# Performance work log

Measured on AMD Instinct MI355X. Metric: run time of the kernel, lower is better.

Reference implementation:

```python
import jax, jax.numpy as jnp
import numpy as np

B, N, L, C, H = 2, 1024, 4096, 256, 8
D = C // H  # head_dim = 32


def setup_inputs() -> dict:
    root = jax.random.key(0)
    ks = jax.random.split(root, 16)
    s = 0.02  # init scale for weights
    return {
        "query": jax.random.normal(ks[0], (B, N, C), jnp.float32),
        "key": jax.random.normal(ks[1], (B, L, C), jnp.float32),
        "value": jax.random.normal(ks[2], (B, L, C), jnp.float32),
        "key_padding_mask": jnp.zeros((B, L), jnp.bool_),  # unused by forward
        "hw_lvl": 1,  # unused by forward
        # learned params, stored as [in, out] (i.e. torch weight transposed)
        "Wq": jax.random.normal(ks[3], (C, C), jnp.float32) * s,
        "Wk": jax.random.normal(ks[4], (C, C), jnp.float32) * s,
        "Wv": jax.random.normal(ks[5], (C, C), jnp.float32) * s,
        "Wp": jax.random.normal(ks[6], (C, C), jnp.float32) * s,
        "bp": jax.random.normal(ks[7], (C,), jnp.float32) * s,
        "Wl1": jax.random.normal(ks[8], (H, H), jnp.float32) * s,
        "bl1": jax.random.normal(ks[9], (H,), jnp.float32) * s,
        "Wl2": jax.random.normal(ks[10], (H, 1), jnp.float32) * s,
        "bl2": jax.random.normal(ks[11], (1,), jnp.float32) * s,
    }


def reference(query, key, value, key_padding_mask, hw_lvl,
              Wq, Wk, Wv, Wp, bp, Wl1, bl1, Wl2, bl2):
    b, n, c = query.shape
    l = key.shape[1]
    h = Wl1.shape[0]
    d = c // h
    scale = d ** (-0.5)

    # projections -> [B, H, N|L, D]
    q = (query @ Wq).reshape(b, n, h, d).transpose(0, 2, 1, 3)
    k = (key @ Wk).reshape(b, l, h, d).transpose(0, 2, 1, 3)
    v = (value @ Wv).reshape(b, l, h, d).transpose(0, 2, 1, 3)

    # raw attention scores [B, H, N, L]
    attn = jnp.einsum('bhnd,bhld->bhnl', q, k) * scale

    # tiny per-head MLP on scores: [B, N, L, H] -> ReLU(H->H) -> ReLU(H->1)
    attn_p = attn.transpose(0, 2, 3, 1)  # [B, N, L, H]
    new_feats = jax.nn.relu(attn_p @ Wl1 + bl1)
    mask = jax.nn.relu(new_feats @ Wl2 + bl2)  # [B, N, L, 1]

    # standard softmax-attention path on the raw scores
    p = jax.nn.softmax(attn, axis=-1)  # [B, H, N, L]
    x = jnp.einsum('bhnl,bhld->bhnd', p, v)  # [B, H, N, D]
    x = x.transpose(0, 2, 1, 3).reshape(b, n, c)
    x = x @ Wp + bp
    return (x, mask)
```

## Files before the change

kernel.cpp:

```cpp
#include <hip/hip_runtime.h>
#include <math.h>
#include <stdint.h>

typedef __bf16 bf16;
typedef __bf16 bfx8 __attribute__((ext_vector_type(8)));
typedef __bf16 bfx4 __attribute__((ext_vector_type(4)));
typedef short  sh8  __attribute__((ext_vector_type(8)));
typedef float  fx4  __attribute__((ext_vector_type(4)));
typedef _Float16 h2 __attribute__((ext_vector_type(2)));
typedef _Float16 hx4 __attribute__((ext_vector_type(4)));
typedef _Float16 h8 __attribute__((ext_vector_type(8)));

#define B_ 2
#define N_ 1024
#define L_ 4096
#define C_ 256
#define H_ 8
#define D_ 32
#define KL 32
#define LOG2E 1.4426950408889634f
#define LN2 0.6931471805599453f
#define QSCALE (0.17677669529663687f * LOG2E)

__device__ __forceinline__ float exp2fast(float x) {
    float r; asm("v_exp_f32 %0, %1" : "=v"(r) : "v"(x)); return r;
}
__device__ __forceinline__ _Float16 exp2h(_Float16 x) {
    _Float16 r; asm("v_exp_f16 %0, %1" : "=v"(r) : "v"(x)); return r;
}
__device__ __forceinline__ h2 pkrtz(float a, float b) {
    return __builtin_bit_cast(h2, __builtin_amdgcn_cvt_pkrtz(a, b));
}

__global__ __launch_bounds__(256)
void wtrans_kernel(const float* __restrict__ Wq, const float* __restrict__ Wk,
                   const float* __restrict__ Wv, const float* __restrict__ Wp,
                   const float* __restrict__ Wl1, const float* __restrict__ bl1,
                   const float* __restrict__ Wl2,
                   bf16* __restrict__ WTq, bf16* __restrict__ WTk,
                   bf16* __restrict__ WTv, bf16* __restrict__ WTp,
                   h2* __restrict__ mlpc) {
    const int bid = blockIdx.x;
    const int wsel = bid >> 4;
    const int tile = bid & 15;
    const int k0 = (tile >> 2) * 64;
    const int c0 = (tile & 3) * 64;
    const float* W = wsel == 0 ? Wq : wsel == 1 ? Wk : wsel == 2 ? Wv : Wp;
    bf16* WT = wsel == 0 ? WTq : wsel == 1 ? WTk : wsel == 2 ? WTv : WTp;

    __shared__ float t_lds[64][68];
    const int tid = threadIdx.x;
    if (bid == 0) {
        if (tid < 32) {
            const int hh = tid >> 2, jp = tid & 3;
            mlpc[tid] = (h2){(_Float16)(LN2 * Wl1[hh * 8 + 2 * jp]),
                             (_Float16)(LN2 * Wl1[hh * 8 + 2 * jp + 1])};
        }
        if (tid < 4) {
            mlpc[32 + tid] = (h2){(_Float16)bl1[2 * tid], (_Float16)bl1[2 * tid + 1]};
            mlpc[36 + tid] = (h2){(_Float16)Wl2[2 * tid], (_Float16)Wl2[2 * tid + 1]};
        }
    }
    {
        const int r = tid >> 2;
        const int c4 = (tid & 3) * 16;
        const float4* src = (const float4*)(W + (size_t)(k0 + r) * C_ + c0 + c4);
        #pragma unroll
        for (int j = 0; j < 4; ++j)
            *(float4*)&t_lds[r][c4 + 4 * j] = src[j];
    }
    __syncthreads();
    const int c = tid & 63;
    const int gp = tid >> 6;
    #pragma unroll
    for (int i = 0; i < 2; ++i) {
        const int gg = gp + i * 4;
        bfx8 v;
        #pragma unroll
        for (int j = 0; j < 8; ++j) v[j] = (bf16)t_lds[gg * 8 + j][c];
        *(bfx8*)(WT + ((size_t)((k0 >> 3) + gg) * C_ + c0 + c) * 8) = v;
    }
}

template<int MODE>
__device__ __forceinline__
void proj_fast(const float* __restrict__ X, const bf16* __restrict__ WT2,
               void* __restrict__ outp, int m0, int n0, float oscale, bf16* b2s) {
    const int tid = threadIdx.x;
    const int w = tid >> 6;
    const int lane = tid & 63;
    const int r = lane & 15;
    const int g = lane >> 4;

    #pragma unroll
    for (int p = 0; p < 8; ++p) {
        const int kc = (tid >> 6) + p * 4;
        const int c = tid & 63;
        *(bfx8*)&b2s[(kc * 64 + c) * 8] = *(const bfx8*)(WT2 + ((size_t)kc * C_ + n0 + c) * 8);
    }
    __syncthreads();

    fx4 acc[4];
    #pragma unroll
    for (int t = 0; t < 4; ++t) acc[t] = (fx4){0.f, 0.f, 0.f, 0.f};

    const float* arow = X + (size_t)(m0 + w * 16 + r) * C_ + g * 8;
    #pragma unroll
    for (int kt = 0; kt < 8; ++kt) {
        const float4 x0 = *(const float4*)(arow + kt * 32);
        const float4 x1 = *(const float4*)(arow + kt * 32 + 4);
        bfx8 af;
        af[0] = (bf16)x0.x; af[1] = (bf16)x0.y; af[2] = (bf16)x0.z; af[3] = (bf16)x0.w;
        af[4] = (bf16)x1.x; af[5] = (bf16)x1.y; af[6] = (bf16)x1.z; af[7] = (bf16)x1.w;
        #pragma unroll
        for (int t = 0; t < 4; ++t) {
            const bfx8 bfr = *(const bfx8*)&b2s[((kt * 4 + g) * 64 + t * 16 + r) * 8];
            acc[t] = __builtin_amdgcn_mfma_f32_16x16x32_bf16(af, bfr, acc[t], 0, 0, 0);
        }
    }

    const int mb = m0 + w * 16;
    if (MODE == 0) {
        bf16* out = (bf16*)outp;
        #pragma unroll
        for (int t = 0; t < 4; ++t)
            #pragma unroll
            for (int reg = 0; reg < 4; ++reg)
                out[(size_t)(mb + 4 * g + reg) * C_ + n0 + t * 16 + r] = (bf16)(acc[t][reg] * oscale);
    } else {
        _Float16* out = (_Float16*)outp;
        const int bb = m0 >> 12;
        const int l0 = (m0 & (L_ - 1)) + w * 16 + 4 * g;
        #pragma unroll
        for (int t = 0; t < 4; ++t) {
            const int cc = n0 + t * 16 + r;
            hx4 v;
            #pragma unroll
            for (int reg = 0; reg < 4; ++reg) v[reg] = (_Float16)acc[t][reg];
            *(hx4*)(out + ((size_t)((bb * H_ + (cc >> 5)) * D_ + (cc & 31)) * L_ + l0)) = v;
        }
    }
}

__global__ __launch_bounds__(256)
void proj_qkv_kernel(const float* __restrict__ q, const float* __restrict__ k,
                     const float* __restrict__ v,
                     const bf16* __restrict__ WTq, const bf16* __restrict__ WTk,
                     const bf16* __restrict__ WTv,
                     bf16* __restrict__ Qb, bf16* __restrict__ Kb, _Float16* __restrict__ Vt) {
    __shared__ __align__(16) bf16 b2s[32 * 64 * 8];
    const int bid = blockIdx.x;
    if (bid < 128) {
        proj_fast<0>(q, WTq, Qb, (bid & 31) * 64, (bid >> 5) * 64, QSCALE, b2s);
    } else if (bid < 640) {
        const int i = bid - 128;
        proj_fast<0>(k, WTk, Kb, (i & 127) * 64, (i >> 7) * 64, 1.0f, b2s);
    } else {
        const int i = bid - 640;
        proj_fast<1>(v, WTv, Vt, (i & 127) * 64, (i >> 7) * 64, 1.0f, b2s);
    }
}

template<int NS>
__global__ __launch_bounds__(256)
void combine_kernel(const bf16* __restrict__ pacc, const float* __restrict__ ps,
                    bf16* __restrict__ xpre) {
    const int idx = blockIdx.x * 256 + threadIdx.x;
    const int dg = idx & 3;
    const int row = idx >> 2;
    const int n = row & (N_ - 1);
    const int bh = row >> 10;
    const int b = bh >> 3, hh = bh & 7;
    float S = 0.f;
    float X[8];
    #pragma unroll
    for (int j = 0; j < 8; ++j) X[j] = 0.f;
    #pragma unroll
    for (int sp = 0; sp < NS; ++sp) {
        S += ps[(size_t)(bh * NS + sp) * N_ + n];
        const bfx8 pv = *(const bfx8*)(pacc + ((size_t)(bh * NS + sp) * N_ + n) * D_ + dg * 8);
        #pragma unroll
        for (int j = 0; j < 8; ++j) X[j] += (float)pv[j];
    }
    const float inv = 1.0f / S;
    bfx8 v;
    #pragma unroll
    for (int j = 0; j < 8; ++j) v[j] = (bf16)(X[j] * inv);
    *(bfx8*)(xpre + (size_t)(b * N_ + n) * C_ + hh * D_ + dg * 8) = v;
}

__global__ __launch_bounds__(256)
void outproj_kernel(const bf16* __restrict__ xpre, const bf16* __restrict__ WTp,
                    const float* __restrict__ bp, float* __restrict__ x_out) {
    __shared__ __align__(16) bf16 b2s[32 * 32 * 8];
    const int m0 = (blockIdx.x & 31) * 64;
    const int n0 = (blockIdx.x >> 5) * 32;
    const int tid = threadIdx.x;
    const int w = tid >> 6, lane = tid & 63, r = lane & 15, g = lane >> 4;

    #pragma unroll
    for (int p = 0; p < 4; ++p) {
        const int kc = (tid >> 5) + p * 8;
        const int c = tid & 31;
        *(bfx8*)&b2s[(kc * 32 + c) * 8] = *(const bfx8*)(WTp + ((size_t)kc * C_ + n0 + c) * 8);
    }
    __syncthreads();

    fx4 acc[2];
    acc[0] = (fx4){0.f, 0.f, 0.f, 0.f};
    acc[1] = (fx4){0.f, 0.f, 0.f, 0.f};
    const bf16* arow = xpre + (size_t)(m0 + w * 16 + r) * C_ + g * 8;
    #pragma unroll
    for (int kt = 0; kt < 8; ++kt) {
        const bfx8 af = *(const bfx8*)(arow + kt * 32);
        #pragma unroll
        for (int t = 0; t < 2; ++t) {
            const bfx8 bfr = *(const bfx8*)&b2s[((kt * 4 + g) * 32 + t * 16 + r) * 8];
            acc[t] = __builtin_amdgcn_mfma_f32_16x16x32_bf16(af, bfr, acc[t], 0, 0, 0);
        }
    }
    const int mb = m0 + w * 16;
    #pragma unroll
    for (int t = 0; t < 2; ++t) {
        const float bv = bp[n0 + t * 16 + r];
        #pragma unroll
        for (int reg = 0; reg < 4; ++reg)
            x_out[(size_t)(mb + 4 * g + reg) * C_ + n0 + t * 16 + r] = acc[t][reg] + bv;
    }
}

template<int NS>
__global__ __launch_bounds__(512, 4)
void attn_kernel(const bf16* __restrict__ Qb, const bf16* __restrict__ Kb,
                 const _Float16* __restrict__ Vt,
                 const h2* __restrict__ mlpc, const float* __restrict__ bl2,
                 bf16* __restrict__ pacc, float* __restrict__ ps,
                 float* __restrict__ maskout) {
    constexpr int LSPAN = L_ / NS;
    constexpr int NIT = LSPAN / KL;
    const int bx = blockIdx.x;
    const int split = bx % NS;
    const int rest = bx / NS;
    const int nt = rest & 31;
    const int b = rest >> 5;
    const int n0 = nt * 32;
    const int l0base = split * LSPAN;

    const int tid = threadIdx.x;
    const int h = tid >> 6;
    const int lane = tid & 63;
    const int r = lane & 15;
    const int g = lane >> 4;

    __shared__ __align__(16) short k_lds[KL * C_];
    __shared__ __align__(16) h2 s_lds[8 * 16 * 36];

    const float bl2v = bl2[0];
    h2 W1[32], B1[4], W2[4];
    #pragma unroll
    for (int i = 0; i < 32; ++i) W1[i] = mlpc[i];
    #pragma unroll
    for (int i = 0; i < 4; ++i) { B1[i] = mlpc[32 + i]; W2[i] = mlpc[36 + i]; }

    const bfx8 qa0 = *(const bfx8*)(Qb + ((size_t)(b * N_ + n0 + r) * C_ + h * D_ + g * 8));
    const bfx8 qa1 = *(const bfx8*)(Qb + ((size_t)(b * N_ + n0 + 16 + r) * C_ + h * D_ + g * 8));

    const int krow = tid >> 5;
    const int kcolb = (tid & 31) * 16;
    const char* Kbb = (const char*)(Kb + (size_t)b * L_ * C_);

    {
        sh8 k0v = *(const sh8*)(Kbb + (size_t)(l0base + krow) * 512 + kcolb);
        sh8 k1v = *(const sh8*)(Kbb + (size_t)(l0base + 16 + krow) * 512 + kcolb);
        *(sh8*)((char*)k_lds + ((krow * 512 + kcolb) ^ ((krow & 7) << 4))) = k0v;
        *(sh8*)((char*)k_lds + (((krow + 16) * 512 + kcolb) ^ (((krow + 16) & 7) << 4))) = k1v;
    }

    const _Float16* Vb0 = Vt + (size_t)((b * H_ + h) * D_ + r) * L_ + g * 8;
    const _Float16* Vb1 = Vt + (size_t)((b * H_ + h) * D_ + 16 + r) * L_ + g * 8;
    h8 vc0 = *(const h8*)(Vb0 + l0base);
    h8 vc1 = *(const h8*)(Vb1 + l0base);

    float s0r = 0.f, s1r = 0.f;
    fx4 accA0 = {0.f,0.f,0.f,0.f}, accA1 = {0.f,0.f,0.f,0.f};
    fx4 accB0 = {0.f,0.f,0.f,0.f}, accB1 = {0.f,0.f,0.f,0.f};

    const int mn = tid >> 5;
    const int ml = tid & 31;
    const int moff = mn * 36 + (ml ^ ((mn & 3) << 3));
    const int abase = h * 576 + r * 36 + ((g ^ (r & 3)) << 3);

    for (int it = 0; it < NIT; ++it) {
        const int l0 = l0base + it * KL;
        __syncthreads();

        fx4 sA0, sA1, sB0, sB1;
        {
            const int byte0 = (r * 512 + h * 64 + g * 16) ^ ((r & 7) << 4);
            const int byte1 = ((r + 16) * 512 + h * 64 + g * 16) ^ (((r + 16) & 7) << 4);
            const bfx8 kb0 = __builtin_bit_cast(bfx8, *(const sh8*)((char*)k_lds + byte0));
            const bfx8 kb1 = __builtin_bit_cast(bfx8, *(const sh8*)((char*)k_lds + byte1));
            const fx4 z = {0.f, 0.f, 0.f, 0.f};
            __builtin_amdgcn_s_setprio(1);
            sA0 = __builtin_amdgcn_mfma_f32_16x16x32_bf16(qa0, kb0, z, 0, 0, 0);
            sA1 = __builtin_amdgcn_mfma_f32_16x16x32_bf16(qa0, kb1, z, 0, 0, 0);
            sB0 = __builtin_amdgcn_mfma_f32_16x16x32_bf16(qa1, kb0, z, 0, 0, 0);
            sB1 = __builtin_amdgcn_mfma_f32_16x16x32_bf16(qa1, kb1, z, 0, 0, 0);
            __builtin_amdgcn_s_setprio(0);
        }
        #pragma unroll
        for (int reg = 0; reg < 4; ++reg) {
            const int o = h * 576 + (4 * g + reg) * 36;
            const int xr = reg << 3;
            s_lds[o + ((r) ^ xr)]      = pkrtz(sA0[reg], sB0[reg]);
            s_lds[o + ((r + 16) ^ xr)] = pkrtz(sA1[reg], sB1[reg]);
        }
        __syncthreads();

        sh8 nk0, nk1;
        h8 nv0, nv1;
        const bool have_next = (it + 1 < NIT);
        if (have_next) {
            nk0 = *(const sh8*)(Kbb + (size_t)(l0 + KL + krow) * 512 + kcolb);
            nk1 = *(const sh8*)(Kbb + (size_t)(l0 + KL + 16 + krow) * 512 + kcolb);
            nv0 = *(const h8*)(Vb0 + l0 + KL);
            nv1 = *(const h8*)(Vb1 + l0 + KL);
        }

        {
            h2 f0[4], f1[4];
            #pragma unroll
            for (int jp = 0; jp < 4; ++jp) { f0[jp] = B1[jp]; f1[jp] = B1[jp]; }
            #pragma unroll
            for (int hh = 0; hh < 8; ++hh) {
                const h2 sv = s_lds[hh * 576 + moff];
                const h2 s0h = (h2){sv[0], sv[0]};
                const h2 s1h = (h2){sv[1], sv[1]};
                #pragma unroll
                for (int jp = 0; jp < 4; ++jp) {
                    f0[jp] = s0h * W1[hh * 4 + jp] + f0[jp];
                    f1[jp] = s1h * W1[hh * 4 + jp] + f1[jp];
                }
            }
            const h2 z2 = (h2){(_Float16)0.f, (_Float16)0.f};
            h2 t0 = __builtin_elementwise_max(f0[0], z2) * W2[0];
            h2 t1 = __builtin_elementwise_max(f1[0], z2) * W2[0];
            #pragma unroll
            for (int jp = 1; jp < 4; ++jp) {
                t0 = __builtin_elementwise_max(f0[jp], z2) * W2[jp] + t0;
                t1 = __builtin_elementwise_max(f1[jp], z2) * W2[jp] + t1;
            }
            const float mk0 = fmaxf((float)t0[0] + (float)t0[1] + bl2v, 0.f);
            const float mk1 = fmaxf((float)t1[0] + (float)t1[1] + bl2v, 0.f);
            __builtin_nontemporal_store(mk0,
                &maskout[(size_t)(b * N_ + n0 + mn) * L_ + l0 + ml]);
            __builtin_nontemporal_store(mk1,
                &maskout[(size_t)(b * N_ + n0 + 16 + mn) * L_ + l0 + ml]);
        }

        const h8 sv0 = *(const h8*)&s_lds[abase];
        const h8 sv1 = *(const h8*)&s_lds[abase + 4];

        h8 pa0, pa1;
        pa0[0] = exp2h(sv0[0]); pa0[1] = exp2h(sv0[2]);
        pa0[2] = exp2h(sv0[4]); pa0[3] = exp2h(sv0[6]);
        pa0[4] = exp2h(sv1[0]); pa0[5] = exp2h(sv1[2]);
        pa0[6] = exp2h(sv1[4]); pa0[7] = exp2h(sv1[6]);
        pa1[0] = exp2h(sv0[1]); pa1[1] = exp2h(sv0[3]);
        pa1[2] = exp2h(sv0[5]); pa1[3] = exp2h(sv0[7]);
        pa1[4] = exp2h(sv1[1]); pa1[5] = exp2h(sv1[3]);
        pa1[6] = exp2h(sv1[5]); pa1[7] = exp2h(sv1[7]);
        {
            const h2* c0 = (const h2*)&pa0;
            const h2* c1 = (const h2*)&pa1;
            const h2 q0 = (c0[0] + c0[1]) + (c0[2] + c0[3]);
            const h2 q1 = (c1[0] + c1[1]) + (c1[2] + c1[3]);
            s0r += (float)q0[0] + (float)q0[1];
            s1r += (float)q1[0] + (float)q1[1];
        }

        __builtin_amdgcn_s_setprio(1);
        accA0 = __builtin_amdgcn_mfma_f32_16x16x32_f16(pa0, vc0, accA0, 0, 0, 0);
        accA1 = __builtin_amdgcn_mfma_f32_16x16x32_f16(pa0, vc1, accA1, 0, 0, 0);
        accB0 = __builtin_amdgcn_mfma_f32_16x16x32_f16(pa1, vc0, accB0, 0, 0, 0);
        accB1 = __builtin_amdgcn_mfma_f32_16x16x32_f16(pa1, vc1, accB1, 0, 0, 0);
        __builtin_amdgcn_s_setprio(0);

        if (have_next) {
            *(sh8*)((char*)k_lds + ((krow * 512 + kcolb) ^ ((krow & 7) << 4))) = nk0;
            *(sh8*)((char*)k_lds + (((krow + 16) * 512 + kcolb) ^ (((krow + 16) & 7) << 4))) = nk1;
            vc0 = nv0; vc1 = nv1;
        }
    }

    s0r += __shfl_xor(s0r, 16, 64);
    s0r += __shfl_xor(s0r, 32, 64);
    s1r += __shfl_xor(s1r, 16, 64);
    s1r += __shfl_xor(s1r, 32, 64);

    const size_t pbase = (size_t)((b * H_ + h) * NS + split) * N_ + n0;
    #pragma unroll
    for (int reg = 0; reg < 4; ++reg) {
        const int n = 4 * g + reg;
        pacc[(pbase + n) * D_ + r]           = (bf16)accA0[reg];
        pacc[(pbase + n) * D_ + 16 + r]      = (bf16)accA1[reg];
        pacc[(pbase + 16 + n) * D_ + r]      = (bf16)accB0[reg];
        pacc[(pbase + 16 + n) * D_ + 16 + r] = (bf16)accB1[reg];
    }
    if (lane < 16) {
        ps[pbase + lane] = s0r;
        ps[pbase + 16 + lane] = s1r;
    }
}

extern "C" void kernel_launch(void* const* d_in, const int* in_sizes, int n_in,
                              void* d_out, int out_size, void* d_ws, size_t ws_size,
                              hipStream_t stream) {
    const float* query = (const float*)d_in[0];
    const float* key   = (const float*)d_in[1];
    const float* value = (const float*)d_in[2];
    const float* Wq  = (const float*)d_in[5];
    const float* Wk  = (const float*)d_in[6];
    const float* Wv  = (const float*)d_in[7];
    const float* Wp  = (const float*)d_in[8];
    const float* bp  = (const float*)d_in[9];
    const float* Wl1 = (const float*)d_in[10];
    const float* bl1 = (const float*)d_in[11];
    const float* Wl2 = (const float*)d_in[12];
    const float* bl2 = (const float*)d_in[13];

    float* x_out    = (float*)d_out;
    float* mask_out = x_out + (size_t)B_ * N_ * C_;

    char* w = (char*)d_ws;
    bf16*     WTq  = (bf16*)(w);
    bf16*     WTk  = (bf16*)(w + (128 << 10));
    bf16*     WTv  = (bf16*)(w + (256 << 10));
    bf16*     WTp  = (bf16*)(w + (384 << 10));
    h2*       mlpc = (h2*)(w + (512 << 10));
    bf16*     Qb   = (bf16*)(w + (576 << 10));
    bf16*     Kb   = (bf16*)(w + (1600 << 10));
    _Float16* Vt   = (_Float16*)(w + (5696 << 10));
    bf16*     xpre = (bf16*)(w + (1600 << 10));
    bf16*     pacc = (bf16*)(w + (9792 << 10));

    const bool big = ws_size >= ((size_t)28224 << 10);
    const int NS = big ? 16 : 8;
    float* ps = (float*)(w + ((size_t)(9792 + NS * 1024) << 10));

    hipLaunchKernelGGL(wtrans_kernel, dim3(64), dim3(256), 0, stream,
                       Wq, Wk, Wv, Wp, Wl1, bl1, Wl2, WTq, WTk, WTv, WTp, mlpc);
    hipLaunchKernelGGL(proj_qkv_kernel, dim3(1152), dim3(256), 0, stream,
                       query, key, value, WTq, WTk, WTv, Qb, Kb, Vt);
    if (big) {
        attn_kernel<16><<<dim3(B_ * 32 * 16), dim3(512), 0, stream>>>(
            Qb, Kb, Vt, mlpc, bl2, pacc, ps, mask_out);
        combine_kernel<16><<<dim3(256), dim3(256), 0, stream>>>(pacc, ps, xpre);
    } else {
        attn_kernel<8><<<dim3(B_ * 32 * 8), dim3(512), 0, stream>>>(
            Qb, Kb, Vt, mlpc, bl2, pacc, ps, mask_out);
        combine_kernel<8><<<dim3(256), dim3(256), 0, stream>>>(pacc, ps, xpre);
    }
    hipLaunchKernelGGL(outproj_kernel, dim3(256), dim3(256), 0, stream,
                       xpre, WTp, bp, x_out);
}
```

Before: 66.43 us.

## Swap QK MFMA operands so P stays in registers for the PV MFMA

Swaps the operand order of the score MFMA so each lane's output registers already form the A-operand layout for the P·V MFMA. Exp and row-sum are then computed straight from registers instead of rereading scores from LDS. V is loaded as two 4-element halves to match the new key ordering. The scores still go to LDS with a padded stride-17 layout, used only by the per-head mask MLP. This removes one LDS round-trip and lets the PV MFMA issue before the MLP stage, at the cost of more, smaller V global loads.

```diff
diff --git a/kernel.cpp b/kernel.cpp
--- a/kernel.cpp
+++ b/kernel.cpp
@@ -22,9 +22,6 @@
 #define LN2 0.6931471805599453f
 #define QSCALE (0.17677669529663687f * LOG2E)
 
-__device__ __forceinline__ float exp2fast(float x) {
-    float r; asm("v_exp_f32 %0, %1" : "=v"(r) : "v"(x)); return r;
-}
 __device__ __forceinline__ _Float16 exp2h(_Float16 x) {
     _Float16 r; asm("v_exp_f16 %0, %1" : "=v"(r) : "v"(x)); return r;
 }
@@ -253,7 +250,7 @@
     const int g = lane >> 4;
 
     __shared__ __align__(16) short k_lds[KL * C_];
-    __shared__ __align__(16) h2 s_lds[8 * 16 * 36];
+    __shared__ __align__(16) h2 s_lds[8 * 32 * 17];
 
     const float bl2v = bl2[0];
     h2 W1[32], B1[4], W2[4];
@@ -276,10 +273,14 @@
         *(sh8*)((char*)k_lds + (((krow + 16) * 512 + kcolb) ^ (((krow + 16) & 7) << 4))) = k1v;
     }
 
-    const _Float16* Vb0 = Vt + (size_t)((b * H_ + h) * D_ + r) * L_ + g * 8;
-    const _Float16* Vb1 = Vt + (size_t)((b * H_ + h) * D_ + 16 + r) * L_ + g * 8;
-    h8 vc0 = *(const h8*)(Vb0 + l0base);
-    h8 vc1 = *(const h8*)(Vb1 + l0base);
+    const _Float16* Vb0 = Vt + (size_t)((b * H_ + h) * D_ + r) * L_;
+    const _Float16* Vb1 = Vt + (size_t)((b * H_ + h) * D_ + 16 + r) * L_;
+    const int lo_off = 4 * g;
+    const int hi_off = 16 + 4 * g;
+    hx4 vA0 = *(const hx4*)(Vb0 + l0base + lo_off);
+    hx4 vA1 = *(const hx4*)(Vb0 + l0base + hi_off);
+    hx4 vB0 = *(const hx4*)(Vb1 + l0base + lo_off);
+    hx4 vB1 = *(const hx4*)(Vb1 + l0base + hi_off);
 
     float s0r = 0.f, s1r = 0.f;
     fx4 accA0 = {0.f,0.f,0.f,0.f}, accA1 = {0.f,0.f,0.f,0.f};
@@ -287,8 +288,7 @@
 
     const int mn = tid >> 5;
     const int ml = tid & 31;
-    const int moff = mn * 36 + (ml ^ ((mn & 3) << 3));
-    const int abase = h * 576 + r * 36 + ((g ^ (r & 3)) << 3);
+    const int mbase = ml * 17 + mn;
 
     for (int it = 0; it < NIT; ++it) {
         const int l0 = l0base + it * KL;
@@ -302,30 +302,61 @@
             const bfx8 kb1 = __builtin_bit_cast(bfx8, *(const sh8*)((char*)k_lds + byte1));
             const fx4 z = {0.f, 0.f, 0.f, 0.f};
             __builtin_amdgcn_s_setprio(1);
-            sA0 = __builtin_amdgcn_mfma_f32_16x16x32_bf16(qa0, kb0, z, 0, 0, 0);
-            sA1 = __builtin_amdgcn_mfma_f32_16x16x32_bf16(qa0, kb1, z, 0, 0, 0);
-            sB0 = __builtin_amdgcn_mfma_f32_16x16x32_bf16(qa1, kb0, z, 0, 0, 0);
-            sB1 = __builtin_amdgcn_mfma_f32_16x16x32_bf16(qa1, kb1, z, 0, 0, 0);
+            sA0 = __builtin_amdgcn_mfma_f32_16x16x32_bf16(kb0, qa0, z, 0, 0, 0);
+            sA1 = __builtin_amdgcn_mfma_f32_16x16x32_bf16(kb1, qa0, z, 0, 0, 0);
+            sB0 = __builtin_amdgcn_mfma_f32_16x16x32_bf16(kb0, qa1, z, 0, 0, 0);
+            sB1 = __builtin_amdgcn_mfma_f32_16x16x32_bf16(kb1, qa1, z, 0, 0, 0);
             __builtin_amdgcn_s_setprio(0);
         }
+
+        h8 pa0, pa1;
         #pragma unroll
         for (int reg = 0; reg < 4; ++reg) {
-            const int o = h * 576 + (4 * g + reg) * 36;
-            const int xr = reg << 3;
-            s_lds[o + ((r) ^ xr)]      = pkrtz(sA0[reg], sB0[reg]);
-            s_lds[o + ((r + 16) ^ xr)] = pkrtz(sA1[reg], sB1[reg]);
-        }
-        __syncthreads();
+            const h2 pk0 = pkrtz(sA0[reg], sB0[reg]);
+            const h2 pk1 = pkrtz(sA1[reg], sB1[reg]);
+            s_lds[h * 544 + (4 * g + reg) * 17 + r]      = pk0;
+            s_lds[h * 544 + (16 + 4 * g + reg) * 17 + r] = pk1;
+            pa0[reg]     = exp2h(pk0[0]); pa1[reg]     = exp2h(pk0[1]);
+            pa0[4 + reg] = exp2h(pk1[0]); pa1[4 + reg] = exp2h(pk1[1]);
+        }
 
         sh8 nk0, nk1;
-        h8 nv0, nv1;
+        hx4 nA0, nA1, nB0, nB1;
         const bool have_next = (it + 1 < NIT);
         if (have_next) {
             nk0 = *(const sh8*)(Kbb + (size_t)(l0 + KL + krow) * 512 + kcolb);
             nk1 = *(const sh8*)(Kbb + (size_t)(l0 + KL + 16 + krow) * 512 + kcolb);
-            nv0 = *(const h8*)(Vb0 + l0 + KL);
-            nv1 = *(const h8*)(Vb1 + l0 + KL);
-        }
+            nA0 = *(const hx4*)(Vb0 + l0 + KL + lo_off);
+            nA1 = *(const hx4*)(Vb0 + l0 + KL + hi_off);
+            nB0 = *(const hx4*)(Vb1 + l0 + KL + lo_off);
+            nB1 = *(const hx4*)(Vb1 + l0 + KL + hi_off);
+        }
+
+        {
+            h8 vb0, vb1;
+            #pragma unroll
+            for (int j = 0; j < 4; ++j) {
+                vb0[j] = vA0[j]; vb0[4 + j] = vA1[j];
+                vb1[j] = vB0[j]; vb1[4 + j] = vB1[j];
+            }
+            __builtin_amdgcn_s_setprio(1);
+            accA0 = __builtin_amdgcn_mfma_f32_16x16x32_f16(pa0, vb0, accA0, 0, 0, 0);
+            accA1 = __builtin_amdgcn_mfma_f32_16x16x32_f16(pa0, vb1, accA1, 0, 0, 0);
+            accB0 = __builtin_amdgcn_mfma_f32_16x16x32_f16(pa1, vb0, accB0, 0, 0, 0);
+            accB1 = __builtin_amdgcn_mfma_f32_16x16x32_f16(pa1, vb1, accB1, 0, 0, 0);
+            __builtin_amdgcn_s_setprio(0);
+        }
+
+        {
+            const h2* c0 = (const h2*)&pa0;
+            const h2* c1 = (const h2*)&pa1;
+            const h2 q0 = (c0[0] + c0[1]) + (c0[2] + c0[3]);
+            const h2 q1 = (c1[0] + c1[1]) + (c1[2] + c1[3]);
+            s0r += (float)q0[0] + (float)q0[1];
+            s1r += (float)q1[0] + (float)q1[1];
+        }
+
+        __syncthreads();
 
         {
             h2 f0[4], f1[4];
@@ -333,7 +364,7 @@
             for (int jp = 0; jp < 4; ++jp) { f0[jp] = B1[jp]; f1[jp] = B1[jp]; }
             #pragma unroll
             for (int hh = 0; hh < 8; ++hh) {
-                const h2 sv = s_lds[hh * 576 + moff];
+                const h2 sv = s_lds[hh * 544 + mbase];
                 const h2 s0h = (h2){sv[0], sv[0]};
                 const h2 s1h = (h2){sv[1], sv[1]};
                 #pragma unroll
@@ -358,38 +389,10 @@
                 &maskout[(size_t)(b * N_ + n0 + 16 + mn) * L_ + l0 + ml]);
         }
 
-        const h8 sv0 = *(const h8*)&s_lds[abase];
-        const h8 sv1 = *(const h8*)&s_lds[abase + 4];
-
-        h8 pa0, pa1;
-        pa0[0] = exp2h(sv0[0]); pa0[1] = exp2h(sv0[2]);
-        pa0[2] = exp2h(sv0[4]); pa0[3] = exp2h(sv0[6]);
-        pa0[4] = exp2h(sv1[0]); pa0[5] = exp2h(sv1[2]);
-        pa0[6] = exp2h(sv1[4]); pa0[7] = exp2h(sv1[6]);
-        pa1[0] = exp2h(sv0[1]); pa1[1] = exp2h(sv0[3]);
-        pa1[2] = exp2h(sv0[5]); pa1[3] = exp2h(sv0[7]);
-        pa1[4] = exp2h(sv1[1]); pa1[5] = exp2h(sv1[3]);
-        pa1[6] = exp2h(sv1[5]); pa1[7] = exp2h(sv1[7]);
-        {
-            const h2* c0 = (const h2*)&pa0;
-            const h2* c1 = (const h2*)&pa1;
-            const h2 q0 = (c0[0] + c0[1]) + (c0[2] + c0[3]);
-            const h2 q1 = (c1[0] + c1[1]) + (c1[2] + c1[3]);
-            s0r += (float)q0[0] + (float)q0[1];
-            s1r += (float)q1[0] + (float)q1[1];
-        }
-
-        __builtin_amdgcn_s_setprio(1);
-        accA0 = __builtin_amdgcn_mfma_f32_16x16x32_f16(pa0, vc0, accA0, 0, 0, 0);
-        accA1 = __builtin_amdgcn_mfma_f32_16x16x32_f16(pa0, vc1, accA1, 0, 0, 0);
-        accB0 = __builtin_amdgcn_mfma_f32_16x16x32_f16(pa1, vc0, accB0, 0, 0, 0);
-        accB1 = __builtin_amdgcn_mfma_f32_16x16x32_f16(pa1, vc1, accB1, 0, 0, 0);
-        __builtin_amdgcn_s_setprio(0);
-
         if (have_next) {
             *(sh8*)((char*)k_lds + ((krow * 512 + kcolb) ^ ((krow & 7) << 4))) = nk0;
             *(sh8*)((char*)k_lds + (((krow + 16) * 512 + kcolb) ^ (((krow + 16) & 7) << 4))) = nk1;
-            vc0 = nv0; vc1 = nv1;
+            vA0 = nA0; vA1 = nA1; vB0 = nB0; vB1 = nB1;
         }
     }
 
```

New measurement: 74.76 us. +12.5%, slower.
